# Kernel optimization log

Measured on AMD Instinct MI355X. Metric: run time of the kernel, lower is better.

Reference implementation:

```python
import jax, jax.numpy as jnp
import numpy as np

N = 512     # nodes
E = 16384   # edges (N * avg_degree 32, unique pairs)
F = 64      # nedgeinput
FO = 64     # nedgeoutput


def setup_inputs() -> dict:
    key = jax.random.key(0)
    ks = jax.random.split(key, 7)
    # unique edge pairs so scatter-assign is well-defined
    perm = jax.random.permutation(ks[0], N * N)[:E]
    edge_index = jnp.stack([perm // N, perm % N]).astype(jnp.int32)  # [2, E]
    C = jax.random.normal(ks[1], (E, F), dtype=jnp.float32)
    batch_node = jax.random.normal(ks[2], (N,), dtype=jnp.float32)
    s = 1.0 / np.sqrt(F)
    W_L1 = jax.random.normal(ks[3], (F, F), dtype=jnp.float32) * s          # Linear(F, F), weight [out,in]
    W_L2 = jax.random.normal(ks[4], (F, F), dtype=jnp.float32) * s
    W_mlp1 = jax.random.normal(ks[5], (8 * F, 2 * F), dtype=jnp.float32) * (1.0 / np.sqrt(2 * F))
    W_mlp2 = jax.random.normal(ks[6], (FO, 8 * F), dtype=jnp.float32) * (1.0 / np.sqrt(8 * F))
    return {"edge_index": edge_index, "C": C, "batch_node": batch_node,
            "W_L1": W_L1, "W_L2": W_L2, "W_mlp1": W_mlp1, "W_mlp2": W_mlp2}


def reference(edge_index, C, batch_node, W_L1, W_L2, W_mlp1, W_mlp2):
    n = batch_node.shape[0]
    f = C.shape[1]
    ei0, ei1 = edge_index[0], edge_index[1]
    X = C @ W_L1.T  # [E, F]  (L1(C))
    Y = C @ W_L2.T  # [E, F]  (L2(C))
    # scatter edges into dense [F, N, N] adjacency-like tensors
    resx = jnp.zeros((f, n, n), dtype=C.dtype).at[:, ei0, ei1].set(X.T)
    resy = jnp.zeros((f, n, n), dtype=C.dtype).at[:, ei0, ei1].set(Y.T)
    # batched dense matmul per feature channel, then gather back at edges
    res = jnp.einsum('fij,fjk->fik', resx, resy)  # [F, N, N]
    tmp_matmul = res[:, ei0, ei1].T  # [E, F]
    tmp = jnp.concatenate([C, tmp_matmul], axis=1)  # [E, 2F]
    return jax.nn.relu(tmp @ W_mlp1.T) @ W_mlp2.T  # [E, FO]
```

## Files before the change

kernel.cpp:

```cpp
#include <hip/hip_runtime.h>

#define NN 512
#define NE 16384
#define NF 64

typedef __attribute__((ext_vector_type(8))) short short8_t;
typedef __attribute__((ext_vector_type(4))) float float4_t;

__device__ inline unsigned short f2bf(float f) {
  unsigned u = __builtin_bit_cast(unsigned, f);
  u += 0x7fff + ((u >> 16) & 1);
  return (unsigned short)(u >> 16);
}
__device__ inline float bf2f(unsigned short u) {
  unsigned v = ((unsigned)u) << 16;
  return __builtin_bit_cast(float, v);
}

__global__ __launch_bounds__(256) void k_xy_mfma(const float* __restrict__ C,
                                                 const float* __restrict__ W1,
                                                 const float* __restrict__ W2,
                                                 const int* __restrict__ ei,
                                                 const float* __restrict__ Wm1,
                                                 const float* __restrict__ Wm2,
                                                 int* __restrict__ eid,
                                                 unsigned* __restrict__ maskO,
                                                 unsigned* __restrict__ maskI,
                                                 unsigned short* __restrict__ Xb,
                                                 unsigned short* __restrict__ Yb,
                                                 unsigned short* __restrict__ W1B,
                                                 unsigned short* __restrict__ W2B) {
  __shared__ __attribute__((aligned(16))) short W1s[64 * 72];
  __shared__ __attribute__((aligned(16))) short W2s[64 * 72];
  int t = threadIdx.x;
  int w = t >> 6;
  int lane = t & 63;
  int col = lane & 15;
  int q = lane >> 4;
  int base_e = blockIdx.x * 64 + w * 16;

  if (t < 64) {
    int e = blockIdx.x * 64 + t;
    int i = ei[e];
    int k = ei[NE + e];
    eid[i * NN + k] = e;
    atomicOr(&maskO[i * 16 + (k >> 5)], 1u << (k & 31));
    atomicOr(&maskI[k * 16 + (i >> 5)], 1u << (i & 31));
  }

  if (t >= 64 && t < 160) {
    int t4 = blockIdx.x * 96 + (t - 64);
    if (t4 < 16384) {
      float4 v = ((const float4*)Wm1)[t4];
      short4 s;
      s.x = f2bf(v.x); s.y = f2bf(v.y); s.z = f2bf(v.z); s.w = f2bf(v.w);
      ((short4*)W1B)[t4] = s;
    } else {
      int i2 = t4 - 16384;
      float4 v = ((const float4*)Wm2)[i2];
      short4 s;
      s.x = f2bf(v.x); s.y = f2bf(v.y); s.z = f2bf(v.z); s.w = f2bf(v.w);
      ((short4*)W2B)[i2] = s;
    }
  }

#pragma unroll
  for (int z = 0; z < 4; z++) {
    int gi = z * 256 + t;
    int r = gi >> 4, c = gi & 15;
    float4 v1 = ((const float4*)W1)[r * 16 + c];
    float4 v2 = ((const float4*)W2)[r * 16 + c];
    short4 s1, s2;
    s1.x = f2bf(v1.x); s1.y = f2bf(v1.y); s1.z = f2bf(v1.z); s1.w = f2bf(v1.w);
    s2.x = f2bf(v2.x); s2.y = f2bf(v2.y); s2.z = f2bf(v2.z); s2.w = f2bf(v2.w);
    *(short4*)(W1s + r * 72 + c * 4) = s1;
    *(short4*)(W2s + r * 72 + c * 4) = s2;
  }
  __syncthreads();

  short8_t bfrag[2];
#pragma unroll
  for (int ks = 0; ks < 2; ks++) {
    float4 c0 = ((const float4*)C)[(size_t)(base_e + col) * 16 + ks * 8 + q * 2];
    float4 c1 = ((const float4*)C)[(size_t)(base_e + col) * 16 + ks * 8 + q * 2 + 1];
    short8_t s;
    s[0] = (short)f2bf(c0.x); s[1] = (short)f2bf(c0.y);
    s[2] = (short)f2bf(c0.z); s[3] = (short)f2bf(c0.w);
    s[4] = (short)f2bf(c1.x); s[5] = (short)f2bf(c1.y);
    s[6] = (short)f2bf(c1.z); s[7] = (short)f2bf(c1.w);
    bfrag[ks] = s;
  }

  float4_t xa[4], ya[4];
#pragma unroll
  for (int ft = 0; ft < 4; ft++) {
    xa[ft] = (float4_t){0.f, 0.f, 0.f, 0.f};
    ya[ft] = (float4_t){0.f, 0.f, 0.f, 0.f};
  }
#pragma unroll
  for (int ks = 0; ks < 2; ks++) {
#pragma unroll
    for (int ft = 0; ft < 4; ft++) {
      short8_t a1 = *(const short8_t*)(W1s + (ft * 16 + col) * 72 + ks * 32 + q * 8);
      short8_t a2 = *(const short8_t*)(W2s + (ft * 16 + col) * 72 + ks * 32 + q * 8);
      xa[ft] = __builtin_amdgcn_mfma_f32_16x16x32_bf16(a1, bfrag[ks], xa[ft], 0, 0, 0);
      ya[ft] = __builtin_amdgcn_mfma_f32_16x16x32_bf16(a2, bfrag[ks], ya[ft], 0, 0, 0);
    }
  }
#pragma unroll
  for (int ft = 0; ft < 4; ft++) {
    short4 sx, sy;
    sx.x = (short)f2bf(xa[ft][0]); sx.y = (short)f2bf(xa[ft][1]);
    sx.z = (short)f2bf(xa[ft][2]); sx.w = (short)f2bf(xa[ft][3]);
    sy.x = (short)f2bf(ya[ft][0]); sy.y = (short)f2bf(ya[ft][1]);
    sy.z = (short)f2bf(ya[ft][2]); sy.w = (short)f2bf(ya[ft][3]);
    *(short4*)(Xb + (size_t)(base_e + col) * 64 + ft * 16 + q * 4) = sx;
    *(short4*)(Yb + (size_t)(base_e + col) * 64 + ft * 16 + q * 4) = sy;
  }
}

__global__ __launch_bounds__(512) void k_spmlp(
    const int* __restrict__ ei,
    const int* __restrict__ eid,
    const unsigned* __restrict__ maskO,
    const unsigned* __restrict__ maskI,
    const unsigned short* __restrict__ Xb,
    const unsigned short* __restrict__ Yb,
    const float* __restrict__ C,
    const unsigned short* __restrict__ W1B,
    const unsigned short* __restrict__ W2B,
    float* __restrict__ out) {
  __shared__ __attribute__((aligned(16))) short W1s[128 * 136];
  __shared__ __attribute__((aligned(16))) short W2s[64 * 136];
  __shared__ __attribute__((aligned(16))) short hS[8][16 * 72];
  __shared__ __attribute__((aligned(16))) short tm[64 * 72];
  __shared__ unsigned short jl16[64][128];

  int t = threadIdx.x;
  int w = t >> 6;
  int lane = t & 63;
  int gl = lane & 15;
  int grp = lane >> 4;

#pragma unroll
  for (int round = 0; round < 2; round++) {
    int le = round * 32 + w * 4 + grp;
    int e = blockIdx.x * 64 + le;
    int i = ei[e];
    int k = ei[NE + e];
    unsigned mm = maskO[i * 16 + gl] & maskI[k * 16 + gl];

    int mcnt = __popc(mm);
    int incl = mcnt;
#pragma unroll
    for (int d = 1; d < 16; d <<= 1) {
      int y = __shfl(incl, (lane & 48) | ((gl - d) & 15));
      if (gl >= d) incl += y;
    }
    int off = incl - mcnt;
    int cnt = __shfl(incl, (lane & 48) | 15);

    unsigned bits = mm;
    while (bits) {
      int b = __builtin_ctz(bits);
      bits &= bits - 1;
      if (off < 128) jl16[le][off] = (unsigned short)(gl * 32 + b);
      off++;
    }
    if (cnt > 128) cnt = 128;

    float acc0 = 0.f, acc1 = 0.f, acc2 = 0.f, acc3 = 0.f;
    for (int base = 0; base < cnt; base += 8) {
      int b = gl & 7;
      int t2 = base + b;
      int jj = jl16[le][t2 < cnt ? t2 : base];
      int addr = (gl < 8) ? (i * NN + jj) : (jj * NN + k);
      int sv = eid[addr];
      short4 xs[8], ys[8];
#pragma unroll
      for (int b2 = 0; b2 < 8; b2++) {
        int s1 = __shfl(sv, (lane & 48) | b2);
        int s2 = __shfl(sv, (lane & 48) | (8 + b2));
        xs[b2] = *(const short4*)(Xb + (size_t)s1 * 64 + gl * 4);
        ys[b2] = *(const short4*)(Yb + (size_t)s2 * 64 + gl * 4);
      }
#pragma unroll
      for (int b2 = 0; b2 < 8; b2++) {
        if (base + b2 < cnt) {
          acc0 = fmaf(bf2f((unsigned short)xs[b2].x), bf2f((unsigned short)ys[b2].x), acc0);
          acc1 = fmaf(bf2f((unsigned short)xs[b2].y), bf2f((unsigned short)ys[b2].y), acc1);
          acc2 = fmaf(bf2f((unsigned short)xs[b2].z), bf2f((unsigned short)ys[b2].z), acc2);
          acc3 = fmaf(bf2f((unsigned short)xs[b2].w), bf2f((unsigned short)ys[b2].w), acc3);
        }
      }
    }
    short4 o4;
    o4.x = (short)f2bf(acc0);
    o4.y = (short)f2bf(acc1);
    o4.z = (short)f2bf(acc2);
    o4.w = (short)f2bf(acc3);
    *(short4*)(tm + le * 72 + gl * 4) = o4;
  }
  __syncthreads();

  int u = w >> 2;
  int wl = w & 3;
  int g = wl & 1;
  int h = wl >> 1;
  int col = lane & 15;
  int q = lane >> 4;
  int base_e = blockIdx.x * 64 + u * 32 + g * 16;
  int le0 = u * 32 + g * 16 + col;

  short8_t btmp[4];
#pragma unroll
  for (int ks = 0; ks < 2; ks++) {
    float4 c0 = ((const float4*)C)[(size_t)(base_e + col) * 16 + ks * 8 + q * 2];
    float4 c1 = ((const float4*)C)[(size_t)(base_e + col) * 16 + ks * 8 + q * 2 + 1];
    short8_t s;
    s[0] = (short)f2bf(c0.x); s[1] = (short)f2bf(c0.y);
    s[2] = (short)f2bf(c0.z); s[3] = (short)f2bf(c0.w);
    s[4] = (short)f2bf(c1.x); s[5] = (short)f2bf(c1.y);
    s[6] = (short)f2bf(c1.z); s[7] = (short)f2bf(c1.w);
    btmp[ks] = s;
  }
#pragma unroll
  for (int ks = 2; ks < 4; ks++)
    btmp[ks] = *(const short8_t*)(tm + le0 * 72 + (ks - 2) * 32 + q * 8);

  float4_t oacc[4];
#pragma unroll
  for (int ft = 0; ft < 4; ft++) oacc[ft] = (float4_t){0.f, 0.f, 0.f, 0.f};

  for (int it = 0; it < 4; it++) {
    __syncthreads();
    {
      uint4* d1 = (uint4*)W1s;
      const uint4* s1 = (const uint4*)W1B;
#pragma unroll
      for (int z = 0; z < 4; z++) {
        int gi = z * 512 + t;
        int r = gi >> 4, c = gi & 15;
        int grow = ((r >> 6) * 4 + it) * 64 + (r & 63);
        d1[r * 17 + c] = s1[(size_t)grow * 16 + c];
      }
      uint4* d2 = (uint4*)W2s;
      const uint4* s2 = (const uint4*)W2B;
#pragma unroll
      for (int z = 0; z < 2; z++) {
        int gi = z * 512 + t;
        int r = gi >> 4, c = gi & 15;
        int gc = ((c >> 3) * 4 + it) * 8 + (c & 7);
        d2[r * 17 + c] = s2[(size_t)r * 64 + gc];
      }
    }
    __syncthreads();

#pragma unroll
    for (int ht = 0; ht < 4; ht++) {
      float4_t hacc = (float4_t){0.f, 0.f, 0.f, 0.f};
#pragma unroll
      for (int ks = 0; ks < 4; ks++) {
        short8_t af = *(const short8_t*)(W1s + (h * 64 + ht * 16 + col) * 136 + ks * 32 + q * 8);
        hacc = __builtin_amdgcn_mfma_f32_16x16x32_bf16(af, btmp[ks], hacc, 0, 0, 0);
      }
      short4 hp;
      hp.x = (short)f2bf(fmaxf(hacc[0], 0.f));
      hp.y = (short)f2bf(fmaxf(hacc[1], 0.f));
      hp.z = (short)f2bf(fmaxf(hacc[2], 0.f));
      hp.w = (short)f2bf(fmaxf(hacc[3], 0.f));
      *(short4*)(&hS[w][col * 72 + ht * 16 + q * 4]) = hp;
    }

#pragma unroll
    for (int ks2 = 0; ks2 < 2; ks2++) {
      short8_t a2 = *(const short8_t*)(&hS[w][col * 72 + ks2 * 32 + q * 8]);
#pragma unroll
      for (int ft = 0; ft < 4; ft++) {
        short8_t b2 = *(const short8_t*)(W2s + (ft * 16 + col) * 136 + h * 64 + ks2 * 32 + q * 8);
        oacc[ft] = __builtin_amdgcn_mfma_f32_16x16x32_bf16(a2, b2, oacc[ft], 0, 0, 0);
      }
    }
  }

  __syncthreads();
  float* red = (float*)W1s;
  if (h == 1) {
#pragma unroll
    for (int ft = 0; ft < 4; ft++)
#pragma unroll
      for (int r = 0; r < 4; r++)
        red[(u * 32 + g * 16 + q * 4 + r) * 66 + ft * 16 + col] = oacc[ft][r];
  }
  __syncthreads();
  if (h == 0) {
#pragma unroll
    for (int ft = 0; ft < 4; ft++)
#pragma unroll
      for (int r = 0; r < 4; r++) {
        float v = oacc[ft][r] + red[(u * 32 + g * 16 + q * 4 + r) * 66 + ft * 16 + col];
        out[(size_t)(base_e + q * 4 + r) * 64 + ft * 16 + col] = v;
      }
  }
}

extern "C" void kernel_launch(void* const* d_in, const int* in_sizes, int n_in,
                              void* d_out, int out_size, void* d_ws, size_t ws_size,
                              hipStream_t stream) {
  const int* ei = (const int*)d_in[0];
  const float* C = (const float*)d_in[1];
  const float* W1 = (const float*)d_in[3];
  const float* W2 = (const float*)d_in[4];
  const float* Wm1 = (const float*)d_in[5];
  const float* Wm2 = (const float*)d_in[6];
  float* out = (float*)d_out;

  char* p = (char*)d_ws;
  int* eid = (int*)p;                 p += (size_t)NN * NN * 4;
  unsigned* masks = (unsigned*)p;     p += (size_t)16384 * 4;
  unsigned short* Xb = (unsigned short*)p;    p += (size_t)NE * NF * 2;
  unsigned short* Yb = (unsigned short*)p;    p += (size_t)NE * NF * 2;
  unsigned short* W1B = (unsigned short*)p;   p += (size_t)512 * 128 * 2;
  unsigned short* W2B = (unsigned short*)p;   p += (size_t)64 * 512 * 2;
  unsigned* maskO = masks;
  unsigned* maskI = masks + 8192;

  hipMemsetAsync(masks, 0, 16384 * sizeof(unsigned), stream);
  k_xy_mfma<<<NE / 64, 256, 0, stream>>>(C, W1, W2, ei, Wm1, Wm2, eid,
                                         maskO, maskI, Xb, Yb, W1B, W2B);
  k_spmlp<<<NE / 64, 512, 0, stream>>>(ei, eid, maskO, maskI, Xb, Yb,
                                       C, W1B, W2B, out);
}
```

Measured before the change: 91.07 us.

## Interleave two edges' sparse gathers, prefetch weights, reuse hS for neighbor lists

```diff
diff --git a/kernel.cpp b/kernel.cpp
--- a/kernel.cpp
+++ b/kernel.cpp
@@ -119,6 +119,34 @@
   }
 }
 
+#define STAGE(it) { \
+    uint4* d1 = (uint4*)W1s; const uint4* s1g = (const uint4*)W1B; \
+    _Pragma("unroll") for (int z = 0; z < 4; z++) { \
+      int gi = z * 512 + t; int r = gi >> 4, c = gi & 15; \
+      int grow = ((r >> 6) * 4 + (it)) * 64 + (r & 63); \
+      d1[r * 17 + c] = s1g[(size_t)grow * 16 + c]; } \
+    uint4* d2 = (uint4*)W2s; const uint4* s2g = (const uint4*)W2B; \
+    _Pragma("unroll") for (int z = 0; z < 2; z++) { \
+      int gi = z * 512 + t; int r = gi >> 4, c = gi & 15; \
+      int gc = ((c >> 3) * 4 + (it)) * 8 + (c & 7); \
+      d2[r * 17 + c] = s2g[(size_t)r * 64 + gc]; } }
+
+#define REMBATCH(le, ii, kk, cnt, ac) { \
+    int t2 = base + b; \
+    int jj = jlbase[(le) * 32 + (t2 < (cnt) ? t2 : base)] & 511; \
+    int sv = eid[(gl < 8) ? ((ii) * NN + jj) : (jj * NN + (kk))]; \
+    short4 xs[8], ys[8]; \
+    _Pragma("unroll") for (int b2 = 0; b2 < 8; b2++) { \
+      int s1 = __shfl(sv, (lane & 48) | b2); \
+      int s2 = __shfl(sv, (lane & 48) | (8 + b2)); \
+      xs[b2] = *(const short4*)(Xb + (size_t)s1 * 64 + gl * 4); \
+      ys[b2] = *(const short4*)(Yb + (size_t)s2 * 64 + gl * 4); } \
+    _Pragma("unroll") for (int b2 = 0; b2 < 8; b2++) if (base + b2 < (cnt)) { \
+      ac[0] = fmaf(bf2f((unsigned short)xs[b2].x), bf2f((unsigned short)ys[b2].x), ac[0]); \
+      ac[1] = fmaf(bf2f((unsigned short)xs[b2].y), bf2f((unsigned short)ys[b2].y), ac[1]); \
+      ac[2] = fmaf(bf2f((unsigned short)xs[b2].z), bf2f((unsigned short)ys[b2].z), ac[2]); \
+      ac[3] = fmaf(bf2f((unsigned short)xs[b2].w), bf2f((unsigned short)ys[b2].w), ac[3]); } }
+
 __global__ __launch_bounds__(512) void k_spmlp(
     const int* __restrict__ ei,
     const int* __restrict__ eid,
@@ -134,74 +162,13 @@
   __shared__ __attribute__((aligned(16))) short W2s[64 * 136];
   __shared__ __attribute__((aligned(16))) short hS[8][16 * 72];
   __shared__ __attribute__((aligned(16))) short tm[64 * 72];
-  __shared__ unsigned short jl16[64][128];
 
   int t = threadIdx.x;
   int w = t >> 6;
   int lane = t & 63;
   int gl = lane & 15;
   int grp = lane >> 4;
-
-#pragma unroll
-  for (int round = 0; round < 2; round++) {
-    int le = round * 32 + w * 4 + grp;
-    int e = blockIdx.x * 64 + le;
-    int i = ei[e];
-    int k = ei[NE + e];
-    unsigned mm = maskO[i * 16 + gl] & maskI[k * 16 + gl];
-
-    int mcnt = __popc(mm);
-    int incl = mcnt;
-#pragma unroll
-    for (int d = 1; d < 16; d <<= 1) {
-      int y = __shfl(incl, (lane & 48) | ((gl - d) & 15));
-      if (gl >= d) incl += y;
-    }
-    int off = incl - mcnt;
-    int cnt = __shfl(incl, (lane & 48) | 15);
-
-    unsigned bits = mm;
-    while (bits) {
-      int b = __builtin_ctz(bits);
-      bits &= bits - 1;
-      if (off < 128) jl16[le][off] = (unsigned short)(gl * 32 + b);
-      off++;
-    }
-    if (cnt > 128) cnt = 128;
-
-    float acc0 = 0.f, acc1 = 0.f, acc2 = 0.f, acc3 = 0.f;
-    for (int base = 0; base < cnt; base += 8) {
-      int b = gl & 7;
-      int t2 = base + b;
-      int jj = jl16[le][t2 < cnt ? t2 : base];
-      int addr = (gl < 8) ? (i * NN + jj) : (jj * NN + k);
-      int sv = eid[addr];
-      short4 xs[8], ys[8];
-#pragma unroll
-      for (int b2 = 0; b2 < 8; b2++) {
-        int s1 = __shfl(sv, (lane & 48) | b2);
-        int s2 = __shfl(sv, (lane & 48) | (8 + b2));
-        xs[b2] = *(const short4*)(Xb + (size_t)s1 * 64 + gl * 4);
-        ys[b2] = *(const short4*)(Yb + (size_t)s2 * 64 + gl * 4);
-      }
-#pragma unroll
-      for (int b2 = 0; b2 < 8; b2++) {
-        if (base + b2 < cnt) {
-          acc0 = fmaf(bf2f((unsigned short)xs[b2].x), bf2f((unsigned short)ys[b2].x), acc0);
-          acc1 = fmaf(bf2f((unsigned short)xs[b2].y), bf2f((unsigned short)ys[b2].y), acc1);
-          acc2 = fmaf(bf2f((unsigned short)xs[b2].z), bf2f((unsigned short)ys[b2].z), acc2);
-          acc3 = fmaf(bf2f((unsigned short)xs[b2].w), bf2f((unsigned short)ys[b2].w), acc3);
-        }
-      }
-    }
-    short4 o4;
-    o4.x = (short)f2bf(acc0);
-    o4.y = (short)f2bf(acc1);
-    o4.z = (short)f2bf(acc2);
-    o4.w = (short)f2bf(acc3);
-    *(short4*)(tm + le * 72 + gl * 4) = o4;
-  }
-  __syncthreads();
+  unsigned short* jlbase = (unsigned short*)hS;
 
   int u = w >> 2;
   int wl = w & 3;
@@ -210,13 +177,107 @@
   int col = lane & 15;
   int q = lane >> 4;
   int base_e = blockIdx.x * 64 + u * 32 + g * 16;
-  int le0 = u * 32 + g * 16 + col;
+  int lem = u * 32 + g * 16 + col;
+
+  int le0 = w * 4 + grp;
+  int le1 = 32 + w * 4 + grp;
+  int e0 = blockIdx.x * 64 + le0;
+  int e1 = blockIdx.x * 64 + le1;
+  int i0 = ei[e0], k0 = ei[NE + e0];
+  int i1 = ei[e1], k1 = ei[NE + e1];
+
+  float4 craw[4];
+#pragma unroll
+  for (int ks = 0; ks < 2; ks++) {
+    craw[2 * ks]     = ((const float4*)C)[(size_t)(base_e + col) * 16 + ks * 8 + q * 2];
+    craw[2 * ks + 1] = ((const float4*)C)[(size_t)(base_e + col) * 16 + ks * 8 + q * 2 + 1];
+  }
+  STAGE(0);
+
+  unsigned mm0 = maskO[i0 * 16 + gl] & maskI[k0 * 16 + gl];
+  unsigned mm1 = maskO[i1 * 16 + gl] & maskI[k1 * 16 + gl];
+
+  int cnt0, cnt1;
+#pragma unroll
+  for (int round = 0; round < 2; round++) {
+    unsigned mm = round ? mm1 : mm0;
+    int le = round ? le1 : le0;
+    int mcnt = __popc(mm);
+    int incl = mcnt;
+#pragma unroll
+    for (int d = 1; d < 16; d <<= 1) {
+      int y = __shfl(incl, (lane & 48) | ((gl - d) & 15));
+      if (gl >= d) incl += y;
+    }
+    int off = incl - mcnt;
+    int cnt = __shfl(incl, (lane & 48) | 15);
+    unsigned bits = mm;
+    while (bits) {
+      int bb = __builtin_ctz(bits);
+      bits &= bits - 1;
+      if (off < 32) jlbase[le * 32 + off] = (unsigned short)(gl * 32 + bb);
+      off++;
+    }
+    if (cnt > 32) cnt = 32;
+    if (round) cnt1 = cnt; else cnt0 = cnt;
+  }
+
+  int b = gl & 7;
+  float ac0[4] = {0.f, 0.f, 0.f, 0.f}, ac1[4] = {0.f, 0.f, 0.f, 0.f};
+  {
+    int jj0 = jlbase[le0 * 32 + (b < cnt0 ? b : 0)] & 511;
+    int jj1 = jlbase[le1 * 32 + (b < cnt1 ? b : 0)] & 511;
+    int sv0 = (cnt0 > 0) ? eid[(gl < 8) ? (i0 * NN + jj0) : (jj0 * NN + k0)] : 0;
+    int sv1 = (cnt1 > 0) ? eid[(gl < 8) ? (i1 * NN + jj1) : (jj1 * NN + k1)] : 0;
+    short4 xs0[8], ys0[8], xs1[8], ys1[8];
+#pragma unroll
+    for (int b2 = 0; b2 < 8; b2++) {
+      int s1 = __shfl(sv0, (lane & 48) | b2);
+      int s2 = __shfl(sv0, (lane & 48) | (8 + b2));
+      xs0[b2] = *(const short4*)(Xb + (size_t)s1 * 64 + gl * 4);
+      ys0[b2] = *(const short4*)(Yb + (size_t)s2 * 64 + gl * 4);
+    }
+#pragma unroll
+    for (int b2 = 0; b2 < 8; b2++) {
+      int s1 = __shfl(sv1, (lane & 48) | b2);
+      int s2 = __shfl(sv1, (lane & 48) | (8 + b2));
+      xs1[b2] = *(const short4*)(Xb + (size_t)s1 * 64 + gl * 4);
+      ys1[b2] = *(const short4*)(Yb + (size_t)s2 * 64 + gl * 4);
+    }
+#pragma unroll
+    for (int b2 = 0; b2 < 8; b2++) if (b2 < cnt0) {
+      ac0[0] = fmaf(bf2f((unsigned short)xs0[b2].x), bf2f((unsigned short)ys0[b2].x), ac0[0]);
+      ac0[1] = fmaf(bf2f((unsigned short)xs0[b2].y), bf2f((unsigned short)ys0[b2].y), ac0[1]);
+      ac0[2] = fmaf(bf2f((unsigned short)xs0[b2].z), bf2f((unsigned short)ys0[b2].z), ac0[2]);
+      ac0[3] = fmaf(bf2f((unsigned short)xs0[b2].w), bf2f((unsigned short)ys0[b2].w), ac0[3]);
+    }
+#pragma unroll
+    for (int b2 = 0; b2 < 8; b2++) if (b2 < cnt1) {
+      ac1[0] = fmaf(bf2f((unsigned short)xs1[b2].x), bf2f((unsigned short)ys1[b2].x), ac1[0]);
+      ac1[1] = fmaf(bf2f((unsigned short)xs1[b2].y), bf2f((unsigned short)ys1[b2].y), ac1[1]);
+      ac1[2] = fmaf(bf2f((unsigned short)xs1[b2].z), bf2f((unsigned short)ys1[b2].z), ac1[2]);
+      ac1[3] = fmaf(bf2f((unsigned short)xs1[b2].w), bf2f((unsigned short)ys1[b2].w), ac1[3]);
+    }
+  }
+  for (int base = 8; base < cnt0; base += 8) REMBATCH(le0, i0, k0, cnt0, ac0);
+  for (int base = 8; base < cnt1; base += 8) REMBATCH(le1, i1, k1, cnt1, ac1);
+
+  {
+    short4 o0, o1;
+    o0.x = (short)f2bf(ac0[0]); o0.y = (short)f2bf(ac0[1]);
+    o0.z = (short)f2bf(ac0[2]); o0.w = (short)f2bf(ac0[3]);
+    o1.x = (short)f2bf(ac1[0]); o1.y = (short)f2bf(ac1[1]);
+    o1.z = (short)f2bf(ac1[2]); o1.w = (short)f2bf(ac1[3]);
+    *(short4*)(tm + le0 * 72 + gl * 4) = o0;
+    *(short4*)(tm + le1 * 72 + gl * 4) = o1;
+  }
+
+  __syncthreads();
 
   short8_t btmp[4];
 #pragma unroll
   for (int ks = 0; ks < 2; ks++) {
-    float4 c0 = ((const float4*)C)[(size_t)(base_e + col) * 16 + ks * 8 + q * 2];
-    float4 c1 = ((const float4*)C)[(size_t)(base_e + col) * 16 + ks * 8 + q * 2 + 1];
+    float4 c0 = craw[2 * ks], c1 = craw[2 * ks + 1];
     short8_t s;
     s[0] = (short)f2bf(c0.x); s[1] = (short)f2bf(c0.y);
     s[2] = (short)f2bf(c0.z); s[3] = (short)f2bf(c0.w);
@@ -226,36 +287,13 @@
   }
 #pragma unroll
   for (int ks = 2; ks < 4; ks++)
-    btmp[ks] = *(const short8_t*)(tm + le0 * 72 + (ks - 2) * 32 + q * 8);
+    btmp[ks] = *(const short8_t*)(tm + lem * 72 + (ks - 2) * 32 + q * 8);
 
   float4_t oacc[4];
 #pragma unroll
   for (int ft = 0; ft < 4; ft++) oacc[ft] = (float4_t){0.f, 0.f, 0.f, 0.f};
 
   for (int it = 0; it < 4; it++) {
-    __syncthreads();
-    {
-      uint4* d1 = (uint4*)W1s;
-      const uint4* s1 = (const uint4*)W1B;
-#pragma unroll
-      for (int z = 0; z < 4; z++) {
-        int gi = z * 512 + t;
-        int r = gi >> 4, c = gi & 15;
-        int grow = ((r >> 6) * 4 + it) * 64 + (r & 63);
-        d1[r * 17 + c] = s1[(size_t)grow * 16 + c];
-      }
-      uint4* d2 = (uint4*)W2s;
-      const uint4* s2 = (const uint4*)W2B;
-#pragma unroll
-      for (int z = 0; z < 2; z++) {
-        int gi = z * 512 + t;
-        int r = gi >> 4, c = gi & 15;
-        int gc = ((c >> 3) * 4 + it) * 8 + (c & 7);
-        d2[r * 17 + c] = s2[(size_t)r * 64 + gc];
-      }
-    }
-    __syncthreads();
-
 #pragma unroll
     for (int ht = 0; ht < 4; ht++) {
       float4_t hacc = (float4_t){0.f, 0.f, 0.f, 0.f};
@@ -281,6 +319,12 @@
         oacc[ft] = __builtin_amdgcn_mfma_f32_16x16x32_bf16(a2, b2, oacc[ft], 0, 0, 0);
       }
     }
+
+    if (it < 3) {
+      __syncthreads();
+      STAGE(it + 1);
+      __syncthreads();
+    }
   }
 
   __syncthreads();
```

Result: faster. 88.34 us (-3.0%).
